# Optimization experiments

Measured on AMD Instinct MI355X. Metric: run time of the kernel, lower is better.

Reference implementation:

```python
import jax, jax.numpy as jnp
import numpy as np

N = 50000   # nodes
E = 800000  # edges (avg degree 16)
F = 64      # n_feat
P = 20      # pos_enc (RWPE dim)
H = 64      # n_hidden
G = 500     # graphs in batch (100 nodes each)


def setup_inputs() -> dict:
    key = jax.random.key(0)
    ks = jax.random.split(key, 32)
    w = lambda k, s: jax.random.normal(k, s, jnp.float32) * 0.05
    inp = {
        "x": jax.random.normal(ks[0], (N, F), jnp.float32),
        "RWPE": jax.random.normal(ks[1], (N, P), jnp.float32),
        "W_rw": w(ks[2], (P, F)), "b_rw": jnp.zeros((F,), jnp.float32),
    }
    for i in range(5):
        din = F if i == 0 else H
        inp[f"Wc{i+1}"] = w(ks[3 + i], (din, H))
        inp[f"bc{i+1}"] = jnp.zeros((H,), jnp.float32)
        inp[f"Wp{i+1}"] = w(ks[8 + i], (din, H))
        inp[f"bp{i+1}"] = jnp.zeros((H,), jnp.float32)
    inp["gamma"] = jnp.ones((H,), jnp.float32)
    inp["beta"] = jnp.zeros((H,), jnp.float32)
    inp["edge_index"] = jax.random.randint(ks[14], (2, E), 0, N, jnp.int32)
    inp["ptr"] = (jnp.arange(G + 1, dtype=jnp.int32) * (N // G))
    return inp


def _gcn_conv(h, W, b, src, dst, dinv):
    # GCNConv: symmetric-normalized aggregation with self-loops, then bias.
    h = h @ W                                             # [N, H]
    msg = h[src] * (dinv[src] * dinv[dst])[:, None]       # [E, H]
    agg = jax.ops.segment_sum(msg, dst, num_segments=N)
    agg = agg + h * (dinv * dinv)[:, None]                # self-loop term
    return agg + b


def reference(x, RWPE, W_rw, b_rw,
              Wc1, bc1, Wc2, bc2, Wc3, bc3, Wc4, bc4, Wc5, bc5,
              Wp1, bp1, Wp2, bp2, Wp3, bp3, Wp4, bp4, Wp5, bp5,
              gamma, beta, edge_index, ptr):
    src, dst = edge_index[0], edge_index[1]
    deg = jax.ops.segment_sum(jnp.ones((E,), jnp.float32), dst, num_segments=N) + 1.0
    dinv = jax.lax.rsqrt(deg)

    pe = RWPE @ W_rw + b_rw                               # Linear_RW
    h = x + pe
    h = jax.nn.relu(_gcn_conv(h, Wc1, bc1, src, dst, dinv))
    # memory_error branch: LapPE = zeros -> no-op add
    convs = [(Wc2, bc2), (Wc3, bc3), (Wc4, bc4), (Wc5, bc5)]
    conps = [(Wp1, bp1), (Wp2, bp2), (Wp3, bp3), (Wp4, bp4)]
    for (Wc, bc), (Wp, bp) in zip(convs, conps):
        pe = jax.nn.relu(_gcn_conv(pe, Wp, bp, src, dst, dinv))
        h = h + pe
        h = _gcn_conv(h, Wc, bc, src, dst, dinv)
        if (Wc is not Wc5):
            h = jax.nn.relu(h)
    # conv5 output goes through BatchNorm1d (training stats) then relu
    mu = jnp.mean(h, axis=0)
    var = jnp.var(h, axis=0)
    h = (h - mu) * jax.lax.rsqrt(var + 1e-5) * gamma + beta
    h = jax.nn.relu(h)
    # segment_csr mean pooling over ptr
    counts = ptr[1:] - ptr[:-1]
    seg = jnp.repeat(jnp.arange(G, dtype=jnp.int32), counts, total_repeat_length=N)
    pooled = jax.ops.segment_sum(h, seg, num_segments=G)
    return pooled / counts[:, None].astype(h.dtype)
```

## Files before the change

### kernel.cpp

```cpp
#include <hip/hip_runtime.h>
#include <hip/hip_fp16.h>

#define NN 50000
#define NE 800000
#define FD 64
#define PD 20
#define NG 500


__global__ void k_deg(const int* __restrict__ dst, int* __restrict__ deg) {
    int e = blockIdx.x * 256 + threadIdx.x;
    if (e < NE) atomicAdd(&deg[dst[e]], 1);
}

__global__ void k_dinv(const int* __restrict__ deg, float* __restrict__ dinv) {
    int i = blockIdx.x * 256 + threadIdx.x;
    if (i < NN) dinv[i] = rsqrtf((float)deg[i] + 1.0f);
}

__global__ void k_scan1(const int* __restrict__ deg, int* __restrict__ rowp, int* __restrict__ bsum) {
    __shared__ int lds[256];
    int t = threadIdx.x;
    int idx = blockIdx.x * 256 + t;
    int v = (idx < NN) ? deg[idx] : 0;
    lds[t] = v;
    __syncthreads();
    for (int off = 1; off < 256; off <<= 1) {
        int add = (t >= off) ? lds[t - off] : 0;
        __syncthreads();
        lds[t] += add;
        __syncthreads();
    }
    if (idx < NN) rowp[idx + 1] = lds[t];
    if (t == 255) bsum[blockIdx.x] = lds[255];
}

__global__ void k_scan2(int* bsum, int nB) {
    __shared__ int lds[256];
    int t = threadIdx.x;
    lds[t] = (t < nB) ? bsum[t] : 0;
    __syncthreads();
    for (int off = 1; off < 256; off <<= 1) {
        int add = (t >= off) ? lds[t - off] : 0;
        __syncthreads();
        lds[t] += add;
        __syncthreads();
    }
    if (t < nB) bsum[t] = lds[t];
}

__global__ void k_scan3(int* __restrict__ rowp, const int* __restrict__ bsum) {
    int idx = blockIdx.x * 256 + threadIdx.x;
    if (idx == 0) rowp[0] = 0;
    if (blockIdx.x > 0 && idx < NN) rowp[idx + 1] += bsum[blockIdx.x - 1];
}

__global__ void k_fill_init(const int* __restrict__ rowp, int* __restrict__ fill) {
    int i = blockIdx.x * 256 + threadIdx.x;
    if (i < NN) fill[i] = rowp[i];
}

__global__ void k_csr_fill(const int* __restrict__ srcA, const int* __restrict__ dstA,
                           const float* __restrict__ dinv,
                           int* __restrict__ fill, int2* __restrict__ meta) {
    int e = blockIdx.x * 256 + threadIdx.x;
    if (e < NE) {
        int s = srcA[e], d = dstA[e];
        int pos = atomicAdd(&fill[d], 1);
        int2 m;
        m.x = s;
        m.y = __float_as_int(dinv[s]);
        meta[pos] = m;
    }
}


__global__ void k_pe(const float* __restrict__ x, const float* __restrict__ rwpe,
                     const float* __restrict__ Wrw, const float* __restrict__ brw,
                     __half* __restrict__ outI) {
    __shared__ float Wl[PD * FD];
    __shared__ float rows[4 * PD];
    int t = threadIdx.x;
    int nodeBase = blockIdx.x * 4;
    for (int i = t; i < PD * FD; i += 256) Wl[i] = Wrw[i];
    if (t < 4 * PD) {
        int n = nodeBase + t / PD;
        rows[t] = (n < NN) ? rwpe[n * PD + (t % PD)] : 0.f;
    }
    __syncthreads();
    int f = t & 63, sl = t >> 6;
    int node = nodeBase + sl;
    if (node < NN) {
        float acc = brw[f];
        #pragma unroll
        for (int k = 0; k < PD; k++) acc += rows[sl * PD + k] * Wl[k * FD + f];
        outI[(size_t)node * 128 + f]      = __float2half_rn(x[node * FD + f] + acc);
        outI[(size_t)node * 128 + 64 + f] = __float2half_rn(acc);
    }
}

__device__ inline void acc8(float* acc, uint4 v, float w) {
    const __half2* h = reinterpret_cast<const __half2*>(&v);
    float2 f0 = __half22float2(h[0]);
    float2 f1 = __half22float2(h[1]);
    float2 f2 = __half22float2(h[2]);
    float2 f3 = __half22float2(h[3]);
    acc[0] += w * f0.x; acc[1] += w * f0.y;
    acc[2] += w * f1.x; acc[3] += w * f1.y;
    acc[4] += w * f2.x; acc[5] += w * f2.y;
    acc[6] += w * f3.x; acc[7] += w * f3.y;
}

__device__ inline void acc4(float* acc, uint2 v, float w) {
    const __half2* h = reinterpret_cast<const __half2*>(&v);
    float2 f0 = __half22float2(h[0]);
    float2 f1 = __half22float2(h[1]);
    acc[0] += w * f0.x; acc[1] += w * f0.y;
    acc[2] += w * f1.x; acc[3] += w * f1.y;
}

template <bool FINAL>
__global__ __launch_bounds__(256) void k_dual(
    const __half* __restrict__ in,
    const float* __restrict__ dinv, const int* __restrict__ rowp,
    const int2* __restrict__ meta,
    const float* __restrict__ Wc, const float* __restrict__ bc,
    const float* __restrict__ Wp, const float* __restrict__ bp,
    __half* __restrict__ out, int write_pe,
    float* __restrict__ foutF)
{
    __shared__ float Wl[64 * 64];
    __shared__ float aggH[16 * 68];
    __shared__ float aggP[16 * 68];
    int t = threadIdx.x;

    {
        const float4* W4 = reinterpret_cast<const float4*>(Wc);
        float4* Wl4 = reinterpret_cast<float4*>(Wl);
        #pragma unroll
        for (int i = 0; i < 4; i++) Wl4[t + 256 * i] = W4[t + 256 * i];
    }

    int l = t & 15;
    int sl = t >> 4;
    int node = blockIdx.x * 16 + sl;
    int e0 = rowp[node], e1 = rowp[node + 1];
    float dd = dinv[node];

    if (!FINAL) {
        const uint4* base = reinterpret_cast<const uint4*>(in);
        float acc[8] = {0, 0, 0, 0, 0, 0, 0, 0};
        int e = e0;
        for (; e + 4 <= e1; e += 4) {
            int2 m0 = meta[e + 0];
            int2 m1 = meta[e + 1];
            int2 m2 = meta[e + 2];
            int2 m3 = meta[e + 3];
            uint4 v0 = base[(size_t)m0.x * 16 + l];
            uint4 v1 = base[(size_t)m1.x * 16 + l];
            uint4 v2 = base[(size_t)m2.x * 16 + l];
            uint4 v3 = base[(size_t)m3.x * 16 + l];
            acc8(acc, v0, __int_as_float(m0.y));
            acc8(acc, v1, __int_as_float(m1.y));
            acc8(acc, v2, __int_as_float(m2.y));
            acc8(acc, v3, __int_as_float(m3.y));
        }
        for (; e < e1; ++e) {
            int2 m = meta[e];
            acc8(acc, base[(size_t)m.x * 16 + l], __int_as_float(m.y));
        }
        float s[8];
        {
            uint4 sv = base[(size_t)node * 16 + l];
            const __half2* h = reinterpret_cast<const __half2*>(&sv);
            float2 f0 = __half22float2(h[0]);
            float2 f1 = __half22float2(h[1]);
            float2 f2 = __half22float2(h[2]);
            float2 f3 = __half22float2(h[3]);
            s[0] = f0.x; s[1] = f0.y; s[2] = f1.x; s[3] = f1.y;
            s[4] = f2.x; s[5] = f2.y; s[6] = f3.x; s[7] = f3.y;
        }
        float* dst = (l < 8) ? &aggH[sl * 68 + l * 8] : &aggP[sl * 68 + (l - 8) * 8];
        float4* d4 = reinterpret_cast<float4*>(dst);
        d4[0] = make_float4(dd * acc[0] + dd * dd * s[0],
                            dd * acc[1] + dd * dd * s[1],
                            dd * acc[2] + dd * dd * s[2],
                            dd * acc[3] + dd * dd * s[3]);
        d4[1] = make_float4(dd * acc[4] + dd * dd * s[4],
                            dd * acc[5] + dd * dd * s[5],
                            dd * acc[6] + dd * dd * s[6],
                            dd * acc[7] + dd * dd * s[7]);
    } else {
        const uint2* base2 = reinterpret_cast<const uint2*>(in);
        float acc[4] = {0, 0, 0, 0};
        int e = e0;
        for (; e + 4 <= e1; e += 4) {
            int2 m0 = meta[e + 0];
            int2 m1 = meta[e + 1];
            int2 m2 = meta[e + 2];
            int2 m3 = meta[e + 3];
            uint2 v0 = base2[(size_t)m0.x * 32 + l];
            uint2 v1 = base2[(size_t)m1.x * 32 + l];
            uint2 v2 = base2[(size_t)m2.x * 32 + l];
            uint2 v3 = base2[(size_t)m3.x * 32 + l];
            acc4(acc, v0, __int_as_float(m0.y));
            acc4(acc, v1, __int_as_float(m1.y));
            acc4(acc, v2, __int_as_float(m2.y));
            acc4(acc, v3, __int_as_float(m3.y));
        }
        for (; e < e1; ++e) {
            int2 m = meta[e];
            acc4(acc, base2[(size_t)m.x * 32 + l], __int_as_float(m.y));
        }
        float s[4];
        {
            uint2 sv = base2[(size_t)node * 32 + l];
            const __half2* h = reinterpret_cast<const __half2*>(&sv);
            float2 f0 = __half22float2(h[0]);
            float2 f1 = __half22float2(h[1]);
            s[0] = f0.x; s[1] = f0.y; s[2] = f1.x; s[3] = f1.y;
        }
        float4* d4 = reinterpret_cast<float4*>(&aggH[sl * 68 + l * 4]);
        d4[0] = make_float4(dd * acc[0] + dd * dd * s[0],
                            dd * acc[1] + dd * dd * s[1],
                            dd * acc[2] + dd * dd * s[2],
                            dd * acc[3] + dd * dd * s[3]);
    }
    __syncthreads();

    int c = t & 15;
    int sl2 = t >> 4;
    int onode = blockIdx.x * 16 + sl2;
    float4 oh = *reinterpret_cast<const float4*>(bc + c * 4);
    {
        const float* arow = &aggH[sl2 * 68];
        #pragma unroll 16
        for (int k = 0; k < 64; k++) {
            float av = arow[k];
            float4 wv = *reinterpret_cast<const float4*>(&Wl[k * 64 + c * 4]);
            oh.x += av * wv.x; oh.y += av * wv.y; oh.z += av * wv.z; oh.w += av * wv.w;
        }
    }
    if (FINAL) {
        *reinterpret_cast<float4*>(foutF + (size_t)onode * 64 + c * 4) = oh;
        return;
    }
    oh.x = fmaxf(oh.x, 0.f); oh.y = fmaxf(oh.y, 0.f);
    oh.z = fmaxf(oh.z, 0.f); oh.w = fmaxf(oh.w, 0.f);

    __syncthreads();
    {
        const float4* W4 = reinterpret_cast<const float4*>(Wp);
        float4* Wl4 = reinterpret_cast<float4*>(Wl);
        #pragma unroll
        for (int i = 0; i < 4; i++) Wl4[t + 256 * i] = W4[t + 256 * i];
    }
    __syncthreads();

    float4 op = *reinterpret_cast<const float4*>(bp + c * 4);
    {
        const float* arow = &aggP[sl2 * 68];
        #pragma unroll 16
        for (int k = 0; k < 64; k++) {
            float av = arow[k];
            float4 wv = *reinterpret_cast<const float4*>(&Wl[k * 64 + c * 4]);
            op.x += av * wv.x; op.y += av * wv.y; op.z += av * wv.z; op.w += av * wv.w;
        }
    }
    op.x = fmaxf(op.x, 0.f); op.y = fmaxf(op.y, 0.f);
    op.z = fmaxf(op.z, 0.f); op.w = fmaxf(op.w, 0.f);

    uint2* out2 = reinterpret_cast<uint2*>(out);
    {
        __half2 a = __floats2half2_rn(oh.x + op.x, oh.y + op.y);
        __half2 b = __floats2half2_rn(oh.z + op.z, oh.w + op.w);
        uint2 u;
        u.x = *reinterpret_cast<unsigned int*>(&a);
        u.y = *reinterpret_cast<unsigned int*>(&b);
        out2[(size_t)onode * 32 + c] = u;
    }
    if (write_pe) {
        __half2 a = __floats2half2_rn(op.x, op.y);
        __half2 b = __floats2half2_rn(op.z, op.w);
        uint2 u;
        u.x = *reinterpret_cast<unsigned int*>(&a);
        u.y = *reinterpret_cast<unsigned int*>(&b);
        out2[(size_t)onode * 32 + 16 + c] = u;
    }
}


__global__ void k_bnstats(const float* __restrict__ h, float* __restrict__ stats) {
    __shared__ float s1[256], s2[256];
    int t = threadIdx.x;
    int f = t & 63, sl = t >> 6;
    float a = 0.f, b = 0.f;
    for (int node = blockIdx.x * 4 + sl; node < NN; node += gridDim.x * 4) {
        float v = h[node * 64 + f];
        a += v;
        b += v * v;
    }
    s1[t] = a;
    s2[t] = b;
    __syncthreads();
    if (t < 64) {
        a = s1[t] + s1[t + 64] + s1[t + 128] + s1[t + 192];
        b = s2[t] + s2[t + 64] + s2[t + 128] + s2[t + 192];
        atomicAdd(&stats[t], a);
        atomicAdd(&stats[64 + t], b);
    }
}

__global__ void k_bnfinal(float* stats) {
    int f = threadIdx.x;
    if (f < 64) {
        float mu = stats[f] / (float)NN;
        float var = stats[64 + f] / (float)NN - mu * mu;
        stats[f] = mu;
        stats[64 + f] = rsqrtf(var + 1e-5f);
    }
}

__global__ void k_pool(const float* __restrict__ h, const float* __restrict__ stats,
                       const float* __restrict__ gamma, const float* __restrict__ beta,
                       const int* __restrict__ ptr, float* __restrict__ out) {
    int g = blockIdx.x;
    int f = threadIdx.x;
    int s = ptr[g], e = ptr[g + 1];
    float mu = stats[f], rstd = stats[64 + f], ga = gamma[f], be = beta[f];
    float acc = 0.f;
    for (int n = s; n < e; n++) {
        float v = (h[n * 64 + f] - mu) * rstd * ga + be;
        acc += fmaxf(v, 0.f);
    }
    out[g * 64 + f] = acc / (float)(e - s);
}


extern "C" void kernel_launch(void* const* d_in, const int* in_sizes, int n_in,
                              void* d_out, int out_size, void* d_ws, size_t ws_size,
                              hipStream_t stream) {
    const float* x    = (const float*)d_in[0];
    const float* rwpe = (const float*)d_in[1];
    const float* Wrw  = (const float*)d_in[2];
    const float* brw  = (const float*)d_in[3];
    const float *Wc[5], *bc[5], *Wp[5], *bp[5];
    for (int i = 0; i < 5; i++) {
        Wc[i] = (const float*)d_in[4 + 4 * i];
        bc[i] = (const float*)d_in[5 + 4 * i];
        Wp[i] = (const float*)d_in[6 + 4 * i];
        bp[i] = (const float*)d_in[7 + 4 * i];
    }
    const float* gamma = (const float*)d_in[24];
    const float* beta  = (const float*)d_in[25];
    const int* ei  = (const int*)d_in[26];
    const int* ptr = (const int*)d_in[27];
    float* out = (float*)d_out;

    char* wsp = (char*)d_ws;
    auto alloc = [&](size_t bytes) { void* p = (void*)wsp; wsp += ((bytes + 255) / 256) * 256; return p; };
    int*    deg   = (int*)alloc(NN * 4);
    int*    rowp  = (int*)alloc((NN + 1) * 4);
    int*    fill  = (int*)alloc(NN * 4);
    int2*   meta  = (int2*)alloc((size_t)NE * 8);
    float*  dinv  = (float*)alloc(NN * 4);
    __half* bufP  = (__half*)alloc((size_t)NN * 128 * 2);
    __half* bufQ  = (__half*)alloc((size_t)NN * 128 * 2);
    float*  bufF  = (float*)alloc((size_t)NN * 64 * 4);
    float*  stats = (float*)alloc(512);
    int*    bsum  = (int*)alloc(256 * 4);

    hipMemsetAsync(deg, 0, NN * 4, stream);
    hipMemsetAsync(stats, 0, 512, stream);

    const int* srcA = ei;
    const int* dstA = ei + NE;

    dim3 b256(256);
    int gE = (NE + 255) / 256;
    int gN = (NN + 255) / 256;
    int gNode16 = NN / 16;

    k_deg<<<gE, b256, 0, stream>>>(dstA, deg);
    k_dinv<<<gN, b256, 0, stream>>>(deg, dinv);
    k_scan1<<<gN, b256, 0, stream>>>(deg, rowp, bsum);
    k_scan2<<<1, b256, 0, stream>>>(bsum, gN);
    k_scan3<<<gN, b256, 0, stream>>>(rowp, bsum);
    k_fill_init<<<gN, b256, 0, stream>>>(rowp, fill);
    k_csr_fill<<<gE, b256, 0, stream>>>(srcA, dstA, dinv, fill, meta);

    k_pe<<<(NN + 3) / 4, b256, 0, stream>>>(x, rwpe, Wrw, brw, bufP);

    k_dual<false><<<gNode16, b256, 0, stream>>>(
        bufP, dinv, rowp, meta, Wc[0], bc[0], Wp[0], bp[0], bufQ, 1, nullptr);
    k_dual<false><<<gNode16, b256, 0, stream>>>(
        bufQ, dinv, rowp, meta, Wc[1], bc[1], Wp[1], bp[1], bufP, 1, nullptr);
    k_dual<false><<<gNode16, b256, 0, stream>>>(
        bufP, dinv, rowp, meta, Wc[2], bc[2], Wp[2], bp[2], bufQ, 1, nullptr);
    k_dual<false><<<gNode16, b256, 0, stream>>>(
        bufQ, dinv, rowp, meta, Wc[3], bc[3], Wp[3], bp[3], bufP, 0, nullptr);
    k_dual<true><<<gNode16, b256, 0, stream>>>(
        bufP, dinv, rowp, meta, Wc[4], bc[4], nullptr, nullptr, nullptr, 0, bufF);

    k_bnstats<<<256, b256, 0, stream>>>(bufF, stats);
    k_bnfinal<<<1, 64, 0, stream>>>(stats);
    k_pool<<<NG, 64, 0, stream>>>(bufF, stats, gamma, beta, ptr, out);
}
```

Measured before the change: 371.2 us.

## Partition CSR fill by XCD dst range, fuse fill init, unroll gathers by 8

CSR construction now launches blocks that each scan a chunk of edges but only handle destinations in a range tied to blockIdx&7. The intent is that fill atomics and meta writes for a given destination range stay on one XCD's L2, assuming round-robin block dispatch across the 8 XCDs. The fill-init kernel is merged into scan3, removing one launch. The aggregation loops in k_dual are unrolled to 8 edges to keep more gathers in flight, at the cost of each edge list being read 8 times during the fill and higher register pressure.

```diff
diff --git a/kernel.cpp b/kernel.cpp
--- a/kernel.cpp
+++ b/kernel.cpp
@@ -6,6 +6,9 @@
 #define FD 64
 #define PD 20
 #define NG 500
+#define NXCD 8
+#define DRANGE 6250
+#define CHUNK_E 2048
 
 
 __global__ void k_deg(const int* __restrict__ dst, int* __restrict__ deg) {
@@ -49,28 +52,36 @@
     if (t < nB) bsum[t] = lds[t];
 }
 
-__global__ void k_scan3(int* __restrict__ rowp, const int* __restrict__ bsum) {
+__global__ void k_scan3(int* __restrict__ rowp, const int* __restrict__ bsum,
+                        int* __restrict__ fill) {
     int idx = blockIdx.x * 256 + threadIdx.x;
-    if (idx == 0) rowp[0] = 0;
-    if (blockIdx.x > 0 && idx < NN) rowp[idx + 1] += bsum[blockIdx.x - 1];
-}
-
-__global__ void k_fill_init(const int* __restrict__ rowp, int* __restrict__ fill) {
-    int i = blockIdx.x * 256 + threadIdx.x;
-    if (i < NN) fill[i] = rowp[i];
-}
-
-__global__ void k_csr_fill(const int* __restrict__ srcA, const int* __restrict__ dstA,
-                           const float* __restrict__ dinv,
-                           int* __restrict__ fill, int2* __restrict__ meta) {
-    int e = blockIdx.x * 256 + threadIdx.x;
-    if (e < NE) {
-        int s = srcA[e], d = dstA[e];
-        int pos = atomicAdd(&fill[d], 1);
-        int2 m;
-        m.x = s;
-        m.y = __float_as_int(dinv[s]);
-        meta[pos] = m;
+    if (idx == 0) { rowp[0] = 0; fill[0] = 0; }
+    if (idx < NN) {
+        int v = rowp[idx + 1];
+        if (blockIdx.x > 0) { v += bsum[blockIdx.x - 1]; rowp[idx + 1] = v; }
+        if (idx + 1 < NN) fill[idx + 1] = v;
+    }
+}
+
+__global__ void k_csr_fill_xcd(const int* __restrict__ srcA, const int* __restrict__ dstA,
+                               const float* __restrict__ dinv,
+                               int* __restrict__ fill, int2* __restrict__ meta) {
+    int xcd = blockIdx.x & 7;
+    int chunk = blockIdx.x >> 3;
+    int lo = xcd * DRANGE;
+    int hi = lo + DRANGE;
+    int base = chunk * CHUNK_E;
+    int end = min(base + CHUNK_E, NE);
+    for (int i = base + threadIdx.x; i < end; i += 256) {
+        int d = dstA[i];
+        if (d >= lo && d < hi) {
+            int s = srcA[i];
+            int pos = atomicAdd(&fill[d], 1);
+            int2 m;
+            m.x = s;
+            m.y = __float_as_int(dinv[s]);
+            meta[pos] = m;
+        }
     }
 }
 
@@ -151,6 +162,32 @@
         const uint4* base = reinterpret_cast<const uint4*>(in);
         float acc[8] = {0, 0, 0, 0, 0, 0, 0, 0};
         int e = e0;
+        for (; e + 8 <= e1; e += 8) {
+            int2 m0 = meta[e + 0];
+            int2 m1 = meta[e + 1];
+            int2 m2 = meta[e + 2];
+            int2 m3 = meta[e + 3];
+            int2 m4 = meta[e + 4];
+            int2 m5 = meta[e + 5];
+            int2 m6 = meta[e + 6];
+            int2 m7 = meta[e + 7];
+            uint4 v0 = base[(size_t)m0.x * 16 + l];
+            uint4 v1 = base[(size_t)m1.x * 16 + l];
+            uint4 v2 = base[(size_t)m2.x * 16 + l];
+            uint4 v3 = base[(size_t)m3.x * 16 + l];
+            uint4 v4 = base[(size_t)m4.x * 16 + l];
+            uint4 v5 = base[(size_t)m5.x * 16 + l];
+            uint4 v6 = base[(size_t)m6.x * 16 + l];
+            uint4 v7 = base[(size_t)m7.x * 16 + l];
+            acc8(acc, v0, __int_as_float(m0.y));
+            acc8(acc, v1, __int_as_float(m1.y));
+            acc8(acc, v2, __int_as_float(m2.y));
+            acc8(acc, v3, __int_as_float(m3.y));
+            acc8(acc, v4, __int_as_float(m4.y));
+            acc8(acc, v5, __int_as_float(m5.y));
+            acc8(acc, v6, __int_as_float(m6.y));
+            acc8(acc, v7, __int_as_float(m7.y));
+        }
         for (; e + 4 <= e1; e += 4) {
             int2 m0 = meta[e + 0];
             int2 m1 = meta[e + 1];
@@ -194,19 +231,31 @@
         const uint2* base2 = reinterpret_cast<const uint2*>(in);
         float acc[4] = {0, 0, 0, 0};
         int e = e0;
-        for (; e + 4 <= e1; e += 4) {
+        for (; e + 8 <= e1; e += 8) {
             int2 m0 = meta[e + 0];
             int2 m1 = meta[e + 1];
             int2 m2 = meta[e + 2];
             int2 m3 = meta[e + 3];
+            int2 m4 = meta[e + 4];
+            int2 m5 = meta[e + 5];
+            int2 m6 = meta[e + 6];
+            int2 m7 = meta[e + 7];
             uint2 v0 = base2[(size_t)m0.x * 32 + l];
             uint2 v1 = base2[(size_t)m1.x * 32 + l];
             uint2 v2 = base2[(size_t)m2.x * 32 + l];
             uint2 v3 = base2[(size_t)m3.x * 32 + l];
+            uint2 v4 = base2[(size_t)m4.x * 32 + l];
+            uint2 v5 = base2[(size_t)m5.x * 32 + l];
+            uint2 v6 = base2[(size_t)m6.x * 32 + l];
+            uint2 v7 = base2[(size_t)m7.x * 32 + l];
             acc4(acc, v0, __int_as_float(m0.y));
             acc4(acc, v1, __int_as_float(m1.y));
             acc4(acc, v2, __int_as_float(m2.y));
             acc4(acc, v3, __int_as_float(m3.y));
+            acc4(acc, v4, __int_as_float(m4.y));
+            acc4(acc, v5, __int_as_float(m5.y));
+            acc4(acc, v6, __int_as_float(m6.y));
+            acc4(acc, v7, __int_as_float(m7.y));
         }
         for (; e < e1; ++e) {
             int2 m = meta[e];
@@ -380,14 +429,14 @@
     int gE = (NE + 255) / 256;
     int gN = (NN + 255) / 256;
     int gNode16 = NN / 16;
+    int gFill = ((NE + CHUNK_E - 1) / CHUNK_E) * 8;
 
     k_deg<<<gE, b256, 0, stream>>>(dstA, deg);
     k_dinv<<<gN, b256, 0, stream>>>(deg, dinv);
     k_scan1<<<gN, b256, 0, stream>>>(deg, rowp, bsum);
     k_scan2<<<1, b256, 0, stream>>>(bsum, gN);
-    k_scan3<<<gN, b256, 0, stream>>>(rowp, bsum);
-    k_fill_init<<<gN, b256, 0, stream>>>(rowp, fill);
-    k_csr_fill<<<gE, b256, 0, stream>>>(srcA, dstA, dinv, fill, meta);
+    k_scan3<<<gN, b256, 0, stream>>>(rowp, bsum, fill);
+    k_csr_fill_xcd<<<gFill, b256, 0, stream>>>(srcA, dstA, dinv, fill, meta);
 
     k_pe<<<(NN + 3) / 4, b256, 0, stream>>>(x, rwpe, Wrw, brw, bufP);
 
```

After: 363.6 us. 1.02x faster.

## Partition degree and CSR-fill atomics by destination range per XCD

Applied to the files above, without the earlier changes.

The degree count and CSR fill kernels now launch 8 blocks per edge chunk, and each block handles only the edges whose destination falls in one of 8 node ranges. The block index low bits pick the range, so each range's atomics should stay on one XCD and its L2 instead of bouncing across dies. In exchange every edge's destination is read eight times. The dinv computation is also folded into scan1 and the fill initialisation into scan3, which removes two small launches.

```diff
diff --git a/kernel.cpp b/kernel.cpp
--- a/kernel.cpp
+++ b/kernel.cpp
@@ -6,23 +6,31 @@
 #define FD 64
 #define PD 20
 #define NG 500
-
-
-__global__ void k_deg(const int* __restrict__ dst, int* __restrict__ deg) {
-    int e = blockIdx.x * 256 + threadIdx.x;
-    if (e < NE) atomicAdd(&deg[dst[e]], 1);
-}
-
-__global__ void k_dinv(const int* __restrict__ deg, float* __restrict__ dinv) {
-    int i = blockIdx.x * 256 + threadIdx.x;
-    if (i < NN) dinv[i] = rsqrtf((float)deg[i] + 1.0f);
-}
-
-__global__ void k_scan1(const int* __restrict__ deg, int* __restrict__ rowp, int* __restrict__ bsum) {
+#define NXCD 8
+#define DRANGE 6250
+#define CHUNK_E 2048
+
+
+__global__ void k_deg_xcd(const int* __restrict__ dstA, int* __restrict__ deg) {
+    int xcd = blockIdx.x & 7;
+    int chunk = blockIdx.x >> 3;
+    int lo = xcd * DRANGE;
+    int hi = lo + DRANGE;
+    int base = chunk * CHUNK_E;
+    int end = min(base + CHUNK_E, NE);
+    for (int i = base + threadIdx.x; i < end; i += 256) {
+        int d = dstA[i];
+        if (d >= lo && d < hi) atomicAdd(&deg[d], 1);
+    }
+}
+
+__global__ void k_scan1(const int* __restrict__ deg, int* __restrict__ rowp,
+                        int* __restrict__ bsum, float* __restrict__ dinv) {
     __shared__ int lds[256];
     int t = threadIdx.x;
     int idx = blockIdx.x * 256 + t;
     int v = (idx < NN) ? deg[idx] : 0;
+    if (idx < NN) dinv[idx] = rsqrtf((float)v + 1.0f);
     lds[t] = v;
     __syncthreads();
     for (int off = 1; off < 256; off <<= 1) {
@@ -49,28 +57,36 @@
     if (t < nB) bsum[t] = lds[t];
 }
 
-__global__ void k_scan3(int* __restrict__ rowp, const int* __restrict__ bsum) {
+__global__ void k_scan3(int* __restrict__ rowp, const int* __restrict__ bsum,
+                        int* __restrict__ fill) {
     int idx = blockIdx.x * 256 + threadIdx.x;
-    if (idx == 0) rowp[0] = 0;
-    if (blockIdx.x > 0 && idx < NN) rowp[idx + 1] += bsum[blockIdx.x - 1];
-}
-
-__global__ void k_fill_init(const int* __restrict__ rowp, int* __restrict__ fill) {
-    int i = blockIdx.x * 256 + threadIdx.x;
-    if (i < NN) fill[i] = rowp[i];
-}
-
-__global__ void k_csr_fill(const int* __restrict__ srcA, const int* __restrict__ dstA,
-                           const float* __restrict__ dinv,
-                           int* __restrict__ fill, int2* __restrict__ meta) {
-    int e = blockIdx.x * 256 + threadIdx.x;
-    if (e < NE) {
-        int s = srcA[e], d = dstA[e];
-        int pos = atomicAdd(&fill[d], 1);
-        int2 m;
-        m.x = s;
-        m.y = __float_as_int(dinv[s]);
-        meta[pos] = m;
+    if (idx == 0) { rowp[0] = 0; fill[0] = 0; }
+    if (idx < NN) {
+        int v = rowp[idx + 1];
+        if (blockIdx.x > 0) { v += bsum[blockIdx.x - 1]; rowp[idx + 1] = v; }
+        if (idx + 1 < NN) fill[idx + 1] = v;
+    }
+}
+
+__global__ void k_csr_fill_xcd(const int* __restrict__ srcA, const int* __restrict__ dstA,
+                               const float* __restrict__ dinv,
+                               int* __restrict__ fill, int2* __restrict__ meta) {
+    int xcd = blockIdx.x & 7;
+    int chunk = blockIdx.x >> 3;
+    int lo = xcd * DRANGE;
+    int hi = lo + DRANGE;
+    int base = chunk * CHUNK_E;
+    int end = min(base + CHUNK_E, NE);
+    for (int i = base + threadIdx.x; i < end; i += 256) {
+        int d = dstA[i];
+        if (d >= lo && d < hi) {
+            int s = srcA[i];
+            int pos = atomicAdd(&fill[d], 1);
+            int2 m;
+            m.x = s;
+            m.y = __float_as_int(dinv[s]);
+            meta[pos] = m;
+        }
     }
 }
 
@@ -377,17 +393,15 @@
     const int* dstA = ei + NE;
 
     dim3 b256(256);
-    int gE = (NE + 255) / 256;
     int gN = (NN + 255) / 256;
     int gNode16 = NN / 16;
-
-    k_deg<<<gE, b256, 0, stream>>>(dstA, deg);
-    k_dinv<<<gN, b256, 0, stream>>>(deg, dinv);
-    k_scan1<<<gN, b256, 0, stream>>>(deg, rowp, bsum);
+    int gFill = ((NE + CHUNK_E - 1) / CHUNK_E) * 8;
+
+    k_deg_xcd<<<gFill, b256, 0, stream>>>(dstA, deg);
+    k_scan1<<<gN, b256, 0, stream>>>(deg, rowp, bsum, dinv);
     k_scan2<<<1, b256, 0, stream>>>(bsum, gN);
-    k_scan3<<<gN, b256, 0, stream>>>(rowp, bsum);
-    k_fill_init<<<gN, b256, 0, stream>>>(rowp, fill);
-    k_csr_fill<<<gE, b256, 0, stream>>>(srcA, dstA, dinv, fill, meta);
+    k_scan3<<<gN, b256, 0, stream>>>(rowp, bsum, fill);
+    k_csr_fill_xcd<<<gFill, b256, 0, stream>>>(srcA, dstA, dinv, fill, meta);
 
     k_pe<<<(NN + 3) / 4, b256, 0, stream>>>(x, rwpe, Wrw, brw, bufP);
 
```

After: 358.1 us. -3.6%, faster.
